# Performance work log

Hardware: AMD Instinct MI355X
Metric: run time of the kernel (lower is better)

## Reference

```python
import jax, jax.numpy as jnp
import numpy as np

B, NQ, NC, DC, DY = 4, 4096, 4096, 2, 8


def setup_inputs() -> dict:
    key = jax.random.key(0)
    k1, k2, k3 = jax.random.split(key, 3)
    x_query = jax.random.normal(k1, (B, NQ, DC), dtype=jnp.float32)
    x_context = jax.random.normal(k2, (B, NC, DC), dtype=jnp.float32)
    y_context = jax.random.normal(k3, (B, NC, DY), dtype=jnp.float32)
    log_length_scale = jnp.asarray(np.log(0.1), dtype=jnp.float32)
    return {
        "x_query": x_query,
        "x_context": x_context,
        "y_context": y_context,
        "log_length_scale": log_length_scale,
    }


def reference(x_query, x_context, y_context, log_length_scale):
    # Squared Euclidean distances: (B, NQ, NC).
    # cdist followed by .pow(2) == squared distance, so compute d2 directly.
    diff = x_query[:, :, None, :] - x_context[:, None, :, :]  # (B,NQ,NC,DC)
    d2 = jnp.sum(diff * diff, axis=-1)                         # (B,NQ,NC)
    length_scale = jnp.exp(log_length_scale)
    weights = jnp.exp(-d2 / (2.0 * length_scale ** 2))         # RBF kernel
    density = jnp.sum(weights, axis=-1, keepdims=True)         # (B,NQ,1)
    weights_norm = weights / (density + 1e-8)
    y_query = jnp.einsum('bqc,bcd->bqd', weights_norm, y_context)  # (B,NQ,DY)
    return jnp.concatenate([y_query, density], axis=-1)        # (B,NQ,DY+1)
```

## Files before the change

### kernel.cpp

```cpp
#include <hip/hip_runtime.h>


#define BB 4
#define NQ 4096
#define NC 4096
#define DY 8
#define NBQ (BB * NQ)

#if __has_builtin(__builtin_amdgcn_exp2f)
#define EXP2F(x) __builtin_amdgcn_exp2f(x)
#else
#define EXP2F(x) exp2f(x)
#endif

typedef short bf16x8 __attribute__((ext_vector_type(8)));
typedef float f32x4  __attribute__((ext_vector_type(4)));

__device__ __forceinline__ short f2bf(float v) {
    return (short)(__builtin_bit_cast(unsigned, v) >> 16);
}
__device__ __forceinline__ unsigned fbits(float v) {
    return __builtin_bit_cast(unsigned, v);
}
__device__ __forceinline__ unsigned bfpair(float w0, float w1) {
#if __has_builtin(__builtin_amdgcn_perm)
    return __builtin_amdgcn_perm(fbits(w1), fbits(w0), 0x07060302u);
#else
    return (fbits(w1) & 0xFFFF0000u) | (fbits(w0) >> 16);
#endif
}

#define GSPLIT 8
#define CCHUNK (NC / GSPLIT)
#define NPAIR (CCHUNK / 2)
#define KSTEPS (CCHUNK / 32)
#define NT 4
#define QPB 256
#define QB (NBQ / QPB)
#define JS ((size_t)GSPLIT * NBQ)
#define WS_FLOATS ((size_t)(DY + 1) * GSPLIT * NBQ)

__global__ __launch_bounds__(256, 4) void setconv_accum_mfma(
    const float* __restrict__ xq, const float* __restrict__ xc,
    const float* __restrict__ yc, const float* __restrict__ lls,
    float* __restrict__ ws)
{
    __shared__ float4 sxp[NPAIR];
    __shared__ float2 shp[NPAIR];
    __shared__ unsigned short yfrag[CCHUNK / 8][16][8];

    const int bid  = blockIdx.x;
    const int gs   = bid & (GSPLIT - 1);
    const int qb   = bid >> 3;
    const int b    = qb >> 4;
    const int tid  = threadIdx.x;
    const int lane = tid & 63;
    const int wv   = tid >> 6;
    const int m    = lane & 15;
    const int quad = lane >> 4;

    const float L    = lls[0];
    const float negk = -0.72134752044448f * EXP2F(L * -2.8853900817779268f);

    {
        const float4* xcp = (const float4*)(((const float2*)xc) + (size_t)b * NC + gs * CCHUNK);
        const float4 v = xcp[tid];
        sxp[tid] = make_float4(v.x, v.z, v.y, v.w);
        shp[tid] = make_float2(negk * fmaf(v.x, v.x, v.y * v.y),
                               negk * fmaf(v.z, v.z, v.w * v.w));
    }
    {
        const float4* yp = (const float4*)(yc + ((size_t)b * NC + gs * CCHUNK) * DY);
#pragma unroll
        for (int i = 0; i < 2; ++i) {
            const int c = tid + 256 * i;
            const float4 A  = yp[2 * c + 0];
            const float4 Bv = yp[2 * c + 1];
            const int g = c >> 3, j = c & 7;
            unsigned short* dst = &yfrag[g][0][j];
            dst[0 * 8] = (unsigned short)f2bf(A.x);
            dst[1 * 8] = (unsigned short)f2bf(A.y);
            dst[2 * 8] = (unsigned short)f2bf(A.z);
            dst[3 * 8] = (unsigned short)f2bf(A.w);
            dst[4 * 8] = (unsigned short)f2bf(Bv.x);
            dst[5 * 8] = (unsigned short)f2bf(Bv.y);
            dst[6 * 8] = (unsigned short)f2bf(Bv.z);
            dst[7 * 8] = (unsigned short)f2bf(Bv.w);
        }
        unsigned* yf32 = (unsigned*)yfrag;
#pragma unroll
        for (int i = 0; i < 8; ++i) {
            const int v = tid + 256 * i;
            const int g2 = v >> 5, r = v & 31;
            yf32[g2 * 64 + 32 + r] = (r < 4) ? 0x3F803F80u : 0u;
        }
    }

    float a0[NT], a1[NT], a2[NT];
#pragma unroll
    for (int t = 0; t < NT; ++t) {
        const int q = qb * QPB + (wv * NT + t) * 16 + m;
        const float2 qv = ((const float2*)xq)[q];
        a0[t] = negk * fmaf(qv.x, qv.x, qv.y * qv.y);
        a1[t] = -2.f * negk * qv.x;
        a2[t] = -2.f * negk * qv.y;
    }

    f32x4 acc[NT];
#pragma unroll
    for (int t = 0; t < NT; ++t) acc[t] = (f32x4){0.f, 0.f, 0.f, 0.f};

    __syncthreads();

#pragma unroll 2
    for (int s = 0; s < KSTEPS; ++s) {
        const int pb = s * 16 + quad * 4;
        const bf16x8 bfrag = *(const bf16x8*)&yfrag[s * 4 + quad][m][0];
        const float4 xpA = sxp[pb + 0]; const float2 hpA = shp[pb + 0];
        const float4 xpB = sxp[pb + 1]; const float2 hpB = shp[pb + 1];
        const float4 xpC = sxp[pb + 2]; const float2 hpC = shp[pb + 2];
        const float4 xpD = sxp[pb + 3]; const float2 hpD = shp[pb + 3];
#pragma unroll
        for (int t = 0; t < NT; ++t) {
            uint4 au;
            {
                float u = fmaf(a2[t], xpA.z, fmaf(a1[t], xpA.x, a0[t] + hpA.x));
                float v = fmaf(a2[t], xpA.w, fmaf(a1[t], xpA.y, a0[t] + hpA.y));
                au.x = bfpair(EXP2F(u), EXP2F(v));
            }
            {
                float u = fmaf(a2[t], xpB.z, fmaf(a1[t], xpB.x, a0[t] + hpB.x));
                float v = fmaf(a2[t], xpB.w, fmaf(a1[t], xpB.y, a0[t] + hpB.y));
                au.y = bfpair(EXP2F(u), EXP2F(v));
            }
            {
                float u = fmaf(a2[t], xpC.z, fmaf(a1[t], xpC.x, a0[t] + hpC.x));
                float v = fmaf(a2[t], xpC.w, fmaf(a1[t], xpC.y, a0[t] + hpC.y));
                au.z = bfpair(EXP2F(u), EXP2F(v));
            }
            {
                float u = fmaf(a2[t], xpD.z, fmaf(a1[t], xpD.x, a0[t] + hpD.x));
                float v = fmaf(a2[t], xpD.w, fmaf(a1[t], xpD.y, a0[t] + hpD.y));
                au.w = bfpair(EXP2F(u), EXP2F(v));
            }
            const bf16x8 af = __builtin_bit_cast(bf16x8, au);
            acc[t] = __builtin_amdgcn_mfma_f32_16x16x32_bf16(af, bfrag, acc[t], 0, 0, 0);
        }
    }

    if (m <= 8) {
        const size_t base = (size_t)m * JS + (size_t)gs * NBQ + (size_t)qb * QPB;
#pragma unroll
        for (int t = 0; t < NT; ++t) {
#pragma unroll
            for (int r = 0; r < 4; ++r)
                ws[base + (wv * NT + t) * 16 + quad * 4 + r] = acc[t][r];
        }
    }
}

__global__ __launch_bounds__(256) void setconv_reduce(
    const float* __restrict__ ws, float* __restrict__ out)
{
    __shared__ float part[4][64][DY + 1];
    const int tid  = threadIdx.x;
    const int qi   = tid & 63;
    const int sg   = tid >> 6;
    const int base = blockIdx.x * 64;
    const int bq   = base + qi;

#pragma unroll
    for (int j = 0; j < DY + 1; ++j) {
        float s = 0.f;
#pragma unroll
        for (int k = 0; k < GSPLIT / 4; ++k) {
            const int split = sg * (GSPLIT / 4) + k;
            s += ws[(size_t)j * JS + (size_t)split * NBQ + bq];
        }
        part[sg][qi][j] = s;
    }
    __syncthreads();

    for (int it = tid; it < 64 * (DY + 1); it += 256) {
        const int q2 = it / (DY + 1);
        const int j  = it - q2 * (DY + 1);
        const float den = part[0][q2][DY] + part[1][q2][DY] +
                          part[2][q2][DY] + part[3][q2][DY];
        float v;
        if (j == DY) {
            v = den;
        } else {
            const float s = part[0][q2][j] + part[1][q2][j] +
                            part[2][q2][j] + part[3][q2][j];
            v = s / (den + 1e-8f);
        }
        out[(size_t)base * (DY + 1) + it] = v;
    }
}

#define FSPLIT 8
#define FCCH (NC / FSPLIT)

__global__ __launch_bounds__(256) void setconv_zero(float4* __restrict__ out) {
    out[blockIdx.x * 256 + threadIdx.x] = make_float4(0.f, 0.f, 0.f, 0.f);
}

__global__ __launch_bounds__(256) void setconv_accum_atomic(
    const float* __restrict__ xq, const float* __restrict__ xc,
    const float* __restrict__ yc, const float* __restrict__ lls,
    float* __restrict__ out)
{
    const int bid   = blockIdx.x;
    const int split = bid & (FSPLIT - 1);
    const int qblk  = (bid / FSPLIT) & (NQ / 256 - 1);
    const int b     = bid / (FSPLIT * (NQ / 256));
    const int q     = qblk * 256 + threadIdx.x;

    const float L    = lls[0];
    const float negk = -0.72134752044448f * EXP2F(L * -2.8853900817779268f);

    const float2 qv = ((const float2*)xq)[b * NQ + q];
    const float qx0 = qv.x, qy0 = qv.y;

    float acc[DY], den = 0.f;
#pragma unroll
    for (int j = 0; j < DY; ++j) acc[j] = 0.f;

    const float2* __restrict__ xcp = ((const float2*)xc) + (size_t)b * NC;
    const float4* __restrict__ ycp = ((const float4*)yc) + (size_t)b * NC * 2;

    const int c0 = split * FCCH;
#pragma unroll 4
    for (int c = c0; c < c0 + FCCH; ++c) {
        const float2 cv = xcp[c];
        const float4 y0 = ycp[2 * c + 0];
        const float4 y1 = ycp[2 * c + 1];
        const float dx = qx0 - cv.x;
        const float dy = qy0 - cv.y;
        const float d2 = fmaf(dy, dy, dx * dx);
        const float w  = EXP2F(d2 * negk);
        den += w;
        acc[0] = fmaf(w, y0.x, acc[0]);
        acc[1] = fmaf(w, y0.y, acc[1]);
        acc[2] = fmaf(w, y0.z, acc[2]);
        acc[3] = fmaf(w, y0.w, acc[3]);
        acc[4] = fmaf(w, y1.x, acc[4]);
        acc[5] = fmaf(w, y1.y, acc[5]);
        acc[6] = fmaf(w, y1.z, acc[6]);
        acc[7] = fmaf(w, y1.w, acc[7]);
    }

    float* o = out + (size_t)(b * NQ + q) * (DY + 1);
#pragma unroll
    for (int j = 0; j < DY; ++j) atomicAdd(o + j, acc[j]);
    atomicAdd(o + DY, den);
}

__global__ __launch_bounds__(256) void setconv_norm(float* __restrict__ out) {
    const int q = blockIdx.x * 256 + threadIdx.x;
    float* o = out + (size_t)q * (DY + 1);
    const float inv = 1.0f / (o[DY] + 1e-8f);
#pragma unroll
    for (int j = 0; j < DY; ++j) o[j] *= inv;
}

extern "C" void kernel_launch(void* const* d_in, const int* in_sizes, int n_in,
                              void* d_out, int out_size, void* d_ws, size_t ws_size,
                              hipStream_t stream) {
    const float* xq  = (const float*)d_in[0];
    const float* xc  = (const float*)d_in[1];
    const float* yc  = (const float*)d_in[2];
    const float* lls = (const float*)d_in[3];
    float* out = (float*)d_out;

    if (ws_size >= WS_FLOATS * sizeof(float)) {
        float* ws = (float*)d_ws;
        setconv_accum_mfma<<<QB * GSPLIT, 256, 0, stream>>>(xq, xc, yc, lls, ws);
        setconv_reduce<<<NBQ / 64, 256, 0, stream>>>(ws, out);
    } else {
        setconv_zero<<<(NBQ * (DY + 1)) / 1024, 256, 0, stream>>>((float4*)out);
        setconv_accum_atomic<<<BB * (NQ / 256) * FSPLIT, 256, 0, stream>>>(xq, xc, yc, lls, out);
        setconv_norm<<<NBQ / 256, 256, 0, stream>>>(out);
    }
}
```

Before: 74.84 us.

## Precompute bf16 y fragments in a prep kernel and halve queries per block

Adds a separate prep kernel that converts y_context to bf16 MFMA B-fragments (with the padded ones-column for density) once into workspace. The accumulate kernel then reads these fragments straight from global memory instead of rebuilding them in shared memory in every block. Queries per block also drop from 256 to 128 (NT 4→2), which doubles the grid and cuts per-block register work. The cost is an extra kernel launch and global loads in the inner loop in place of LDS reads, and the workspace-size check now uses an 8 MB offset.

Result: no change. 74.85 us (+0.0%).

```diff
diff --git a/kernel.cpp b/kernel.cpp
--- a/kernel.cpp
+++ b/kernel.cpp
@@ -34,25 +34,52 @@
 #define CCHUNK (NC / GSPLIT)
 #define NPAIR (CCHUNK / 2)
 #define KSTEPS (CCHUNK / 32)
-#define NT 4
-#define QPB 256
+#define NT 2
+#define QPB 128
 #define QB (NBQ / QPB)
 #define JS ((size_t)GSPLIT * NBQ)
 #define WS_FLOATS ((size_t)(DY + 1) * GSPLIT * NBQ)
+#define BFR_OFF_BYTES (8u << 20)
+#define NGRP (NC / 8)
+
+__global__ __launch_bounds__(256) void setconv_prep(
+    const float* __restrict__ yc, unsigned short* __restrict__ bfG)
+{
+    const int T = blockIdx.x * 256 + threadIdx.x;
+    const int b = T >> 12, c = T & 4095;
+    const int g = c >> 3, j = c & 7;
+    const float4* yp = ((const float4*)yc) + (size_t)(b * NC + c) * 2;
+    const float4 A = yp[0], Bv = yp[1];
+    unsigned short* dst = bfG + (size_t)(b * NGRP + g) * 128 + j;
+    dst[0 * 8] = (unsigned short)f2bf(A.x);
+    dst[1 * 8] = (unsigned short)f2bf(A.y);
+    dst[2 * 8] = (unsigned short)f2bf(A.z);
+    dst[3 * 8] = (unsigned short)f2bf(A.w);
+    dst[4 * 8] = (unsigned short)f2bf(Bv.x);
+    dst[5 * 8] = (unsigned short)f2bf(Bv.y);
+    dst[6 * 8] = (unsigned short)f2bf(Bv.z);
+    dst[7 * 8] = (unsigned short)f2bf(Bv.w);
+    unsigned* y32 = (unsigned*)bfG;
+#pragma unroll
+    for (int i = 0; i < 4; ++i) {
+        const int V = T + 16384 * i;
+        const int bg = V >> 5, r = V & 31;
+        y32[(size_t)bg * 64 + 32 + r] = (r < 4) ? 0x3F803F80u : 0u;
+    }
+}
 
 __global__ __launch_bounds__(256, 4) void setconv_accum_mfma(
     const float* __restrict__ xq, const float* __restrict__ xc,
-    const float* __restrict__ yc, const float* __restrict__ lls,
+    const unsigned short* __restrict__ bfG, const float* __restrict__ lls,
     float* __restrict__ ws)
 {
     __shared__ float4 sxp[NPAIR];
     __shared__ float2 shp[NPAIR];
-    __shared__ unsigned short yfrag[CCHUNK / 8][16][8];
 
     const int bid  = blockIdx.x;
     const int gs   = bid & (GSPLIT - 1);
     const int qb   = bid >> 3;
-    const int b    = qb >> 4;
+    const int b    = qb >> 5;
     const int tid  = threadIdx.x;
     const int lane = tid & 63;
     const int wv   = tid >> 6;
@@ -69,32 +96,6 @@
         shp[tid] = make_float2(negk * fmaf(v.x, v.x, v.y * v.y),
                                negk * fmaf(v.z, v.z, v.w * v.w));
     }
-    {
-        const float4* yp = (const float4*)(yc + ((size_t)b * NC + gs * CCHUNK) * DY);
-#pragma unroll
-        for (int i = 0; i < 2; ++i) {
-            const int c = tid + 256 * i;
-            const float4 A  = yp[2 * c + 0];
-            const float4 Bv = yp[2 * c + 1];
-            const int g = c >> 3, j = c & 7;
-            unsigned short* dst = &yfrag[g][0][j];
-            dst[0 * 8] = (unsigned short)f2bf(A.x);
-            dst[1 * 8] = (unsigned short)f2bf(A.y);
-            dst[2 * 8] = (unsigned short)f2bf(A.z);
-            dst[3 * 8] = (unsigned short)f2bf(A.w);
-            dst[4 * 8] = (unsigned short)f2bf(Bv.x);
-            dst[5 * 8] = (unsigned short)f2bf(Bv.y);
-            dst[6 * 8] = (unsigned short)f2bf(Bv.z);
-            dst[7 * 8] = (unsigned short)f2bf(Bv.w);
-        }
-        unsigned* yf32 = (unsigned*)yfrag;
-#pragma unroll
-        for (int i = 0; i < 8; ++i) {
-            const int v = tid + 256 * i;
-            const int g2 = v >> 5, r = v & 31;
-            yf32[g2 * 64 + 32 + r] = (r < 4) ? 0x3F803F80u : 0u;
-        }
-    }
 
     float a0[NT], a1[NT], a2[NT];
 #pragma unroll
@@ -110,12 +111,14 @@
 #pragma unroll
     for (int t = 0; t < NT; ++t) acc[t] = (f32x4){0.f, 0.f, 0.f, 0.f};
 
+    const unsigned short* bfb = bfG + (size_t)(b * NGRP + gs * (CCHUNK / 8)) * 128;
+
     __syncthreads();
 
 #pragma unroll 2
     for (int s = 0; s < KSTEPS; ++s) {
         const int pb = s * 16 + quad * 4;
-        const bf16x8 bfrag = *(const bf16x8*)&yfrag[s * 4 + quad][m][0];
+        const bf16x8 bfrag = *(const bf16x8*)(bfb + (size_t)(s * 4 + quad) * 128 + m * 8);
         const float4 xpA = sxp[pb + 0]; const float2 hpA = shp[pb + 0];
         const float4 xpB = sxp[pb + 1]; const float2 hpB = shp[pb + 1];
         const float4 xpC = sxp[pb + 2]; const float2 hpC = shp[pb + 2];
@@ -273,9 +276,11 @@
     const float* lls = (const float*)d_in[3];
     float* out = (float*)d_out;
 
-    if (ws_size >= WS_FLOATS * sizeof(float)) {
+    if (ws_size >= BFR_OFF_BYTES + (1u << 20)) {
         float* ws = (float*)d_ws;
-        setconv_accum_mfma<<<QB * GSPLIT, 256, 0, stream>>>(xq, xc, yc, lls, ws);
+        unsigned short* bfG = (unsigned short*)((char*)d_ws + BFR_OFF_BYTES);
+        setconv_prep<<<NBQ / 256, 256, 0, stream>>>(yc, bfG);
+        setconv_accum_mfma<<<QB * GSPLIT, 256, 0, stream>>>(xq, xc, bfG, lls, ws);
         setconv_reduce<<<NBQ / 64, 256, 0, stream>>>(ws, out);
     } else {
         setconv_zero<<<(NBQ * (DY + 1)) / 1024, 256, 0, stream>>>((float4*)out);
```
